# Performance work log

Hardware: AMD Instinct MI355X
Metric: run time of the kernel (lower is better)

The kernel has to match this reference:

```python
import jax, jax.numpy as jnp
import numpy as np

NEG_INF_SCALE = -1e9


def setup_inputs() -> dict:
    key = jax.random.key(0)
    ks = jax.random.split(key, 8)
    B, T, M, D = 64, 1024, 256, 1024
    query = jax.random.normal(ks[0], (B, 1, M), dtype=jnp.float32)
    keys = jax.random.normal(ks[1], (B, T, M), dtype=jnp.float32)
    values = jax.random.normal(ks[2], (B, T, D), dtype=jnp.float32)
    mask = jax.random.randint(ks[3], (B, 1, T), 0, 2).astype(jnp.float32)
    # MLP params (scaled like torch default init ~ 1/sqrt(fan_in))
    W1 = jax.random.normal(ks[4], (4 * M, D), dtype=jnp.float32) / np.sqrt(4 * M)
    b1 = jnp.zeros((D,), dtype=jnp.float32)
    W2 = jax.random.normal(ks[5], (D, D), dtype=jnp.float32) / np.sqrt(D)
    b2 = jnp.zeros((D,), dtype=jnp.float32)
    w_score = jax.random.normal(ks[6], (D, 1), dtype=jnp.float32) / np.sqrt(D)
    b_score = jnp.zeros((1,), dtype=jnp.float32)
    return {"query": query, "keys": keys, "values": values, "mask": mask,
            "W1": W1, "b1": b1, "W2": W2, "b2": b2,
            "w_score": w_score, "b_score": b_score}


def reference(query, keys, values, mask, W1, b1, W2, b2, w_score, b_score):
    # query: [B,1,M] broadcast against keys: [B,T,M]
    q = jnp.broadcast_to(query, keys.shape)
    att_input = jnp.concatenate([q, keys, q - keys, q * keys], axis=-1)  # [B,T,4M]
    h = jax.nn.relu(att_input @ W1 + b1)   # [B,T,D]
    h = jax.nn.relu(h @ W2 + b2)           # [B,T,D]
    score = h @ w_score + b_score          # [B,T,1]
    logits = jnp.swapaxes(score, 1, 2)     # [B,1,T]
    logits = logits + mask * NEG_INF_SCALE
    attn = jax.nn.softmax(logits, axis=-1)  # [B,1,T]
    out = jnp.matmul(attn, values)          # [B,1,D]
    return out
```

## Files before the change

### kernel.cpp

```cpp
#include <hip/hip_runtime.h>

#define DEV __device__ __forceinline__

typedef __attribute__((ext_vector_type(4))) float f32x4;
typedef __attribute__((ext_vector_type(8))) short short8;
typedef __attribute__((ext_vector_type(4))) short s16x4;
typedef __attribute__((ext_vector_type(4))) float f32x4v;

DEV short f2bf(float f) {
  union { float f; unsigned u; } v; v.f = f;
  unsigned r = (v.u + 0x7FFFu + ((v.u >> 16) & 1u)) >> 16;
  return (short)r;
}

DEV void gload16(const void* g, void* l) {
  __builtin_amdgcn_global_load_lds(
      (const __attribute__((address_space(1))) void*)g,
      (__attribute__((address_space(3))) void*)l, 16, 0, 0);
}

#define BAR() __builtin_amdgcn_s_barrier()
#define LGKMW(n)                                              \
  {                                                           \
    asm volatile("s_waitcnt lgkmcnt(" #n ")" ::: "memory");   \
    __builtin_amdgcn_sched_barrier(0);                        \
  }
#define VMW(n)                                                \
  {                                                           \
    asm volatile("s_waitcnt vmcnt(" #n ")" ::: "memory");     \
    __builtin_amdgcn_sched_barrier(0);                        \
  }

#define RD_A(pb, qrt)                                                          \
  _Pragma("unroll") for (int m_ = 0; m_ < 4; ++m_) {                           \
    af[m_][0] = *(const short8*)&lds[(pb) + aoff0 + ((qrt) * 4 + m_) * 1024];  \
    af[m_][1] = *(const short8*)&lds[(pb) + aoff1 + ((qrt) * 4 + m_) * 1024];  \
  }
#define RD_B(pb, nh)                                                             \
  _Pragma("unroll") for (int n_ = 0; n_ < 2; ++n_) {                             \
    bf[nh][n_][0] = *(const short8*)&lds[(pb) + boff0 + ((nh) * 2 + n_) * 1024]; \
    bf[nh][n_][1] = *(const short8*)&lds[(pb) + boff1 + ((nh) * 2 + n_) * 1024]; \
  }
#define MFMA_Q(mq, nh)                                                           \
  __builtin_amdgcn_s_setprio(1);                                                 \
  _Pragma("unroll") for (int m_ = 0; m_ < 4; ++m_) {                             \
    _Pragma("unroll") for (int n_ = 0; n_ < 2; ++n_) {                           \
      acc[(mq) * 4 + m_][(nh) * 2 + n_] =                                        \
          __builtin_amdgcn_mfma_f32_16x16x32_bf16(                               \
              bf[nh][n_][0], af[m_][0], acc[(mq) * 4 + m_][(nh) * 2 + n_], 0, 0, \
              0);                                                                \
      acc[(mq) * 4 + m_][(nh) * 2 + n_] =                                        \
          __builtin_amdgcn_mfma_f32_16x16x32_bf16(                               \
              bf[nh][n_][1], af[m_][1], acc[(mq) * 4 + m_][(nh) * 2 + n_], 0, 0, \
              0);                                                                \
    }                                                                            \
  }                                                                              \
  __builtin_amdgcn_s_setprio(0);

struct FullTag { static constexpr bool value = true; };
struct LastTag { static constexpr bool value = false; };


__global__ __launch_bounds__(256) void k_prep_keys(const float* __restrict__ k,
                                                   short* __restrict__ o) {
  int i = (blockIdx.x * 256 + threadIdx.x) * 8;
  f32x4v v0 = *(const f32x4v*)(k + i);
  f32x4v v1 = *(const f32x4v*)(k + i + 4);
  short8 s;
  s[0] = f2bf(v0[0]); s[1] = f2bf(v0[1]); s[2] = f2bf(v0[2]); s[3] = f2bf(v0[3]);
  s[4] = f2bf(v1[0]); s[5] = f2bf(v1[1]); s[6] = f2bf(v1[2]); s[7] = f2bf(v1[3]);
  *(short8*)(o + i) = s;
}

__global__ __launch_bounds__(256) void k_prep_w2t(const float* __restrict__ w2,
                                                  short* __restrict__ w2t) {
  __shared__ float tile[64][65];
  const int k0 = blockIdx.x * 64, n0 = blockIdx.y * 64;
  const int a = threadIdx.x & 63, q = threadIdx.x >> 6;
#pragma unroll
  for (int i = 0; i < 16; ++i) {
    int kk = i * 4 + q;
    tile[kk][a] = w2[(size_t)(k0 + kk) * 1024 + n0 + a];
  }
  __syncthreads();
#pragma unroll
  for (int i = 0; i < 16; ++i) {
    int nn = i * 4 + q;
    w2t[(size_t)(n0 + nn) * 1024 + k0 + a] = f2bf(tile[a][nn]);
  }
}

__global__ __launch_bounds__(256) void k_prep_wkt(const float* __restrict__ w1,
                                                  const float* __restrict__ query,
                                                  const float* __restrict__ b1,
                                                  short* __restrict__ wkt,
                                                  float* __restrict__ biasb) {
  __shared__ short tile[64][257];
  __shared__ float redm[64][4];
  const int b = blockIdx.x, d0 = blockIdx.y * 64;
  const int d = threadIdx.x & 63, mq = threadIdx.x >> 6;
  float bacc = 0.f;
#pragma unroll 4
  for (int i = 0; i < 64; ++i) {
    int m = i * 4 + mq;
    float qv = query[b * 256 + m];
    float wa = w1[(size_t)m * 1024 + d0 + d];
    float wb = w1[(size_t)(256 + m) * 1024 + d0 + d];
    float wc = w1[(size_t)(512 + m) * 1024 + d0 + d];
    float wd = w1[(size_t)(768 + m) * 1024 + d0 + d];
    tile[d][m] = f2bf(wb - wc + qv * wd);
    bacc += qv * (wa + wc);
  }
  redm[d][mq] = bacc;
  __syncthreads();
  const int m = threadIdx.x;
  for (int dd = 0; dd < 64; ++dd)
    wkt[((size_t)b * 1024 + d0 + dd) * 256 + m] = tile[dd][m];
  if (threadIdx.x < 64) {
    int dd = threadIdx.x;
    biasb[b * 1024 + d0 + dd] =
        redm[dd][0] + redm[dd][1] + redm[dd][2] + redm[dd][3] + b1[d0 + dd];
  }
}


template <int MODE>
__global__ __launch_bounds__(512) void k_gemm8(const short* __restrict__ A,
                                               const short* __restrict__ B,
                                               const float* __restrict__ bias,
                                               const float* __restrict__ wscore,
                                               short* __restrict__ hout,
                                               float* __restrict__ spart) {
  __shared__ short lds[65536];
  constexpr int SK = (MODE == 1) ? 256 : 1024;
  constexpr int KT = (MODE == 1) ? 4 : 16;

  const int tid = threadIdx.x;
  const int bx = blockIdx.x;
  const int L = (bx & 7) * 128 + (bx >> 3);

  const short *Ab, *Bb;
  const float *biasp, *wsp = nullptr;
  short* houtp = nullptr;
  int rt, ct;
  if constexpr (MODE == 1) {
    const int b = L >> 4;
    rt = (L >> 2) & 3; ct = L & 3;
    Ab = A + ((size_t)b * 1024 + rt * 256) * 256;
    Bb = B + ((size_t)b * 1024 + ct * 256) * 256;
    biasp = bias + b * 1024 + ct * 256;
    houtp = hout + ((size_t)(b * 1024 + rt * 256)) * 1024 + ct * 256;
  } else {
    rt = L >> 2; ct = L & 3;
    Ab = A + (size_t)rt * 256 * 1024;
    Bb = B + (size_t)ct * 256 * 1024;
    biasp = bias + ct * 256;
    wsp = wscore + ct * 256;
  }

  const int c0 = tid, c1 = 512 + tid;
  const int r0 = c0 >> 3, k0 = ((c0 & 7) ^ (r0 & 7)) * 8;
  const int r1 = c1 >> 3, k1 = ((c1 & 7) ^ (r1 & 7)) * 8;

  auto STAGE = [&](const short* gb, int kt, int half, int ldsb) {
    gload16(gb + (size_t)(half * 128 + r0) * SK + kt * 64 + k0, &lds[ldsb + c0 * 8]);
    gload16(gb + (size_t)(half * 128 + r1) * SK + kt * 64 + k1, &lds[ldsb + c1 * 8]);
  };

  const int lane = tid & 63, l15 = lane & 15, l4 = lane >> 4;
  const int wid = tid >> 6, wr = wid >> 2, wc = wid & 3;
  const int aoff0 = wr * 8192 + l15 * 64 + ((l4 ^ (l15 & 7)) * 8);
  const int aoff1 = wr * 8192 + l15 * 64 + (((4 + l4) ^ (l15 & 7)) * 8);
  const int boff0 = 16384 + (wc >> 1) * 8192 + (wc & 1) * 4096 + l15 * 64 +
                    ((l4 ^ (l15 & 7)) * 8);
  const int boff1 = 16384 + (wc >> 1) * 8192 + (wc & 1) * 4096 + l15 * 64 +
                    (((4 + l4) ^ (l15 & 7)) * 8);

  f32x4 acc[8][4];
#pragma unroll
  for (int m = 0; m < 8; ++m)
#pragma unroll
    for (int n = 0; n < 4; ++n) acc[m][n] = f32x4{0.f, 0.f, 0.f, 0.f};
  short8 af[4][2];
  short8 bf[2][2][2];

  STAGE(Ab, 0, 0, 0);
  STAGE(Ab, 0, 1, 8192);
  STAGE(Bb, 0, 0, 16384);
  STAGE(Bb, 0, 1, 24576);
  STAGE(Ab, 1, 0, 32768);
  STAGE(Ab, 1, 1, 40960);
  VMW(4);
  BAR();

  auto body = [&](int t, auto tag) {
    constexpr bool FULL = decltype(tag)::value;
    const int p = (t & 1) << 15;
    const int q = p ^ 32768;
    RD_A(p, 0); RD_B(p, 0); RD_B(p, 1);
    STAGE(Bb, t + 1, 0, q + 16384);
    BAR(); LGKMW(4); MFMA_Q(0, 0); BAR();
    STAGE(Bb, t + 1, 1, q + 24576);
    BAR(); LGKMW(0); MFMA_Q(0, 1); BAR();
    RD_A(p, 1);
    if constexpr (FULL) STAGE(Bb, t + 2, 0, p + 16384);
    BAR(); LGKMW(0); MFMA_Q(1, 1); BAR();
    if constexpr (FULL) STAGE(Bb, t + 2, 1, p + 24576);
    BAR();
    MFMA_Q(1, 0);
    if constexpr (FULL) { VMW(4); } else { VMW(0); }
    BAR();
    RD_A(q, 0); RD_B(q, 0); RD_B(q, 1);
    if constexpr (FULL) STAGE(Ab, t + 2, 0, p + 0);
    BAR(); LGKMW(4); MFMA_Q(0, 0); BAR();
    if constexpr (FULL) STAGE(Ab, t + 2, 1, p + 8192);
    BAR(); LGKMW(0); MFMA_Q(0, 1); BAR();
    RD_A(q, 1);
    BAR(); LGKMW(0); MFMA_Q(1, 1); BAR();
    if constexpr (FULL) { STAGE(Ab, t + 3, 0, q + 0); STAGE(Ab, t + 3, 1, q + 8192); }
    BAR();
    MFMA_Q(1, 0);
    if constexpr (FULL) { VMW(4); }
    BAR();
  };

#pragma nounroll
  for (int i = 0; i < KT / 2 - 1; ++i) body(2 * i, FullTag{});
  body(KT - 2, LastTag{});

  if constexpr (MODE == 1) {
    float bv[4][4];
#pragma unroll
    for (int n = 0; n < 4; ++n)
#pragma unroll
      for (int r2 = 0; r2 < 4; ++r2) bv[n][r2] = biasp[wc * 64 + n * 16 + l4 * 4 + r2];
#pragma unroll
    for (int m = 0; m < 8; ++m) {
      int row = wr * 128 + m * 16 + l15;
#pragma unroll
      for (int n = 0; n < 4; ++n) {
        s16x4 pk;
#pragma unroll
        for (int r2 = 0; r2 < 4; ++r2)
          pk[r2] = f2bf(fmaxf(acc[m][n][r2] + bv[n][r2], 0.f));
        *(s16x4*)&houtp[(size_t)row * 1024 + wc * 64 + n * 16 + l4 * 4] = pk;
      }
    }
  } else {
    float bv[4][4], wv[4][4];
#pragma unroll
    for (int n = 0; n < 4; ++n)
#pragma unroll
      for (int r2 = 0; r2 < 4; ++r2) {
        int c = wc * 64 + n * 16 + l4 * 4 + r2;
        bv[n][r2] = biasp[c];
        wv[n][r2] = wsp[c];
      }
    float* so = spart + ((size_t)(ct * 4 + wc) << 16) + rt * 256 + wr * 128;
#pragma unroll
    for (int m = 0; m < 8; ++m) {
      float s = 0.f;
#pragma unroll
      for (int n = 0; n < 4; ++n)
#pragma unroll
        for (int r2 = 0; r2 < 4; ++r2)
          s += fmaxf(acc[m][n][r2] + bv[n][r2], 0.f) * wv[n][r2];
      s += __shfl_xor(s, 16);
      s += __shfl_xor(s, 32);
      if (lane < 16) so[m * 16 + l15] = s;
    }
  }
}


__global__ __launch_bounds__(256) void k_softmax(const float* __restrict__ spart,
                                                 const float* __restrict__ mask,
                                                 const float* __restrict__ bscore,
                                                 float* __restrict__ attn) {
  const int b = blockIdx.x, tid = threadIdx.x;
  __shared__ float sm[1024];
  __shared__ float red[8];
  const float bs = bscore[0];
  float lmax = -3.0e38f;
  for (int t = tid; t < 1024; t += 256) {
    float s = bs;
#pragma unroll
    for (int c = 0; c < 16; ++c) s += spart[(size_t)c * 65536 + b * 1024 + t];
    float lg = s + mask[b * 1024 + t] * (-1e9f);
    sm[t] = lg;
    lmax = fmaxf(lmax, lg);
  }
  for (int o = 32; o; o >>= 1) lmax = fmaxf(lmax, __shfl_xor(lmax, o));
  const int wid = tid >> 6, lane = tid & 63;
  if (lane == 0) red[wid] = lmax;
  __syncthreads();
  float bmax = fmaxf(fmaxf(red[0], red[1]), fmaxf(red[2], red[3]));
  float lsum = 0.f;
  for (int t = tid; t < 1024; t += 256) {
    float e = __expf(sm[t] - bmax);
    sm[t] = e;
    lsum += e;
  }
  for (int o = 32; o; o >>= 1) lsum += __shfl_xor(lsum, o);
  __syncthreads();
  if (lane == 0) red[wid] = lsum;
  __syncthreads();
  float inv = 1.0f / (red[0] + red[1] + red[2] + red[3]);
  for (int t = tid; t < 1024; t += 256) attn[b * 1024 + t] = sm[t] * inv;
}

__global__ __launch_bounds__(256) void k_out(const float* __restrict__ attn,
                                             const float* __restrict__ values,
                                             float* __restrict__ part) {
  const int b = blockIdx.x >> 3, ts = blockIdx.x & 7;
  const int tid = threadIdx.x;
  __shared__ float at[128];
  if (tid < 128) at[tid] = attn[b * 1024 + ts * 128 + tid];
  __syncthreads();
  const float* vb = values + ((size_t)b * 1024 + ts * 128) * 1024 + tid * 4;
  f32x4 acc = {0.f, 0.f, 0.f, 0.f};
#pragma unroll 8
  for (int t = 0; t < 128; ++t) {
    f32x4v v = *(const f32x4v*)(vb + (size_t)t * 1024);
    float a = at[t];
    acc[0] += a * v[0]; acc[1] += a * v[1]; acc[2] += a * v[2]; acc[3] += a * v[3];
  }
  *(f32x4*)(part + ((size_t)(b * 8 + ts)) * 1024 + tid * 4) = acc;
}

__global__ __launch_bounds__(256) void k_red(const float* __restrict__ part,
                                             float* __restrict__ out) {
  const int b = blockIdx.x;
  const int c4 = threadIdx.x * 4;
  f32x4 s = {0.f, 0.f, 0.f, 0.f};
#pragma unroll
  for (int ts = 0; ts < 8; ++ts) {
    f32x4v v = *(const f32x4v*)(part + ((size_t)(b * 8 + ts)) * 1024 + c4);
    s[0] += v[0]; s[1] += v[1]; s[2] += v[2]; s[3] += v[3];
  }
  *(f32x4*)(out + b * 1024 + c4) = s;
}


extern "C" void kernel_launch(void* const* d_in, const int* in_sizes, int n_in,
                              void* d_out, int out_size, void* d_ws, size_t ws_size,
                              hipStream_t stream) {
  const float* query  = (const float*)d_in[0];
  const float* keys   = (const float*)d_in[1];
  const float* values = (const float*)d_in[2];
  const float* mask   = (const float*)d_in[3];
  const float* W1     = (const float*)d_in[4];
  const float* b1     = (const float*)d_in[5];
  const float* W2     = (const float*)d_in[6];
  const float* b2     = (const float*)d_in[7];
  const float* wscore = (const float*)d_in[8];
  const float* bscore = (const float*)d_in[9];
  float* out = (float*)d_out;

  char* ws = (char*)d_ws;
  short* keysb = (short*)(ws);
  short* wkt   = (short*)(ws + 33554432ull);
  short* w2t   = (short*)(ws + 67108864ull);
  float* biasb = (float*)(ws + 69206016ull);
  short* h1    = (short*)(ws + 69468160ull);
  float* spart = (float*)(ws + 203685888ull);
  float* attn  = (float*)(ws + 207880192ull);
  float* part  = (float*)(ws + 208142336ull);

  k_prep_keys<<<8192, 256, 0, stream>>>(keys, keysb);
  k_prep_w2t<<<dim3(16, 16), 256, 0, stream>>>(W2, w2t);
  k_prep_wkt<<<dim3(64, 16), 256, 0, stream>>>(W1, query, b1, wkt, biasb);

  k_gemm8<1><<<1024, 512, 0, stream>>>(keysb, wkt, biasb, nullptr, h1, nullptr);
  k_gemm8<2><<<1024, 512, 0, stream>>>(h1, w2t, b2, wscore, nullptr, spart);

  k_softmax<<<64, 256, 0, stream>>>(spart, mask, bscore, attn);
  k_out<<<512, 256, 0, stream>>>(attn, values, part);
  k_red<<<64, 256, 0, stream>>>(part, out);
}
```

Baseline: 282.7 us.

## Double-buffer fragment registers and reorder GEMM pipeline to overlap LDS reads with MFMA

```diff
diff --git a/kernel.cpp b/kernel.cpp
--- a/kernel.cpp
+++ b/kernel.cpp
@@ -20,6 +20,7 @@
 }
 
 #define BAR() __builtin_amdgcn_s_barrier()
+#define SB0() __builtin_amdgcn_sched_barrier(0)
 #define LGKMW(n)                                              \
   {                                                           \
     asm volatile("s_waitcnt lgkmcnt(" #n ")" ::: "memory");   \
@@ -31,28 +32,28 @@
     __builtin_amdgcn_sched_barrier(0);                        \
   }
 
-#define RD_A(pb, qrt)                                                          \
+#define RD_A(AF, B, qrt)                                                       \
   _Pragma("unroll") for (int m_ = 0; m_ < 4; ++m_) {                           \
-    af[m_][0] = *(const short8*)&lds[(pb) + aoff0 + ((qrt) * 4 + m_) * 1024];  \
-    af[m_][1] = *(const short8*)&lds[(pb) + aoff1 + ((qrt) * 4 + m_) * 1024];  \
-  }
-#define RD_B(pb, nh)                                                             \
+    AF[m_][0] = *(const short8*)&lds[(B) + aoff0 + (qrt) * 4096 + m_ * 1024];  \
+    AF[m_][1] = *(const short8*)&lds[(B) + aoff1 + (qrt) * 4096 + m_ * 1024];  \
+  }
+#define RD_B(BF, B, nh)                                                          \
   _Pragma("unroll") for (int n_ = 0; n_ < 2; ++n_) {                             \
-    bf[nh][n_][0] = *(const short8*)&lds[(pb) + boff0 + ((nh) * 2 + n_) * 1024]; \
-    bf[nh][n_][1] = *(const short8*)&lds[(pb) + boff1 + ((nh) * 2 + n_) * 1024]; \
-  }
-#define MFMA_Q(mq, nh)                                                           \
+    BF[n_][0] = *(const short8*)&lds[(B) + 16384 + (nh) * 8192 + n_ * 4096 +     \
+                                     boff0];                                     \
+    BF[n_][1] = *(const short8*)&lds[(B) + 16384 + (nh) * 8192 + n_ * 4096 +     \
+                                     boff1];                                     \
+  }
+#define MFMA_Q(mq, nh, AF, BF)                                                   \
   __builtin_amdgcn_s_setprio(1);                                                 \
   _Pragma("unroll") for (int m_ = 0; m_ < 4; ++m_) {                             \
     _Pragma("unroll") for (int n_ = 0; n_ < 2; ++n_) {                           \
       acc[(mq) * 4 + m_][(nh) * 2 + n_] =                                        \
           __builtin_amdgcn_mfma_f32_16x16x32_bf16(                               \
-              bf[nh][n_][0], af[m_][0], acc[(mq) * 4 + m_][(nh) * 2 + n_], 0, 0, \
-              0);                                                                \
+              BF[n_][0], AF[m_][0], acc[(mq) * 4 + m_][(nh) * 2 + n_], 0, 0, 0); \
       acc[(mq) * 4 + m_][(nh) * 2 + n_] =                                        \
           __builtin_amdgcn_mfma_f32_16x16x32_bf16(                               \
-              bf[nh][n_][1], af[m_][1], acc[(mq) * 4 + m_][(nh) * 2 + n_], 0, 0, \
-              0);                                                                \
+              BF[n_][1], AF[m_][1], acc[(mq) * 4 + m_][(nh) * 2 + n_], 0, 0, 0); \
     }                                                                            \
   }                                                                              \
   __builtin_amdgcn_s_setprio(0);
@@ -134,6 +135,7 @@
   __shared__ short lds[65536];
   constexpr int SK = (MODE == 1) ? 256 : 1024;
   constexpr int KT = (MODE == 1) ? 4 : 16;
+  constexpr int P = 0, Q = 32768;
 
   const int tid = threadIdx.x;
   const int bx = blockIdx.x;
@@ -171,57 +173,81 @@
   const int wid = tid >> 6, wr = wid >> 2, wc = wid & 3;
   const int aoff0 = wr * 8192 + l15 * 64 + ((l4 ^ (l15 & 7)) * 8);
   const int aoff1 = wr * 8192 + l15 * 64 + (((4 + l4) ^ (l15 & 7)) * 8);
-  const int boff0 = 16384 + (wc >> 1) * 8192 + (wc & 1) * 4096 + l15 * 64 +
-                    ((l4 ^ (l15 & 7)) * 8);
-  const int boff1 = 16384 + (wc >> 1) * 8192 + (wc & 1) * 4096 + l15 * 64 +
-                    (((4 + l4) ^ (l15 & 7)) * 8);
+  const int boff0 = wc * 1024 + l15 * 64 + ((l4 ^ (l15 & 7)) * 8);
+  const int boff1 = wc * 1024 + l15 * 64 + (((4 + l4) ^ (l15 & 7)) * 8);
 
   f32x4 acc[8][4];
 #pragma unroll
   for (int m = 0; m < 8; ++m)
 #pragma unroll
     for (int n = 0; n < 4; ++n) acc[m][n] = f32x4{0.f, 0.f, 0.f, 0.f};
-  short8 af[4][2];
-  short8 bf[2][2][2];
-
-  STAGE(Ab, 0, 0, 0);
-  STAGE(Ab, 0, 1, 8192);
-  STAGE(Bb, 0, 0, 16384);
-  STAGE(Bb, 0, 1, 24576);
-  STAGE(Ab, 1, 0, 32768);
-  STAGE(Ab, 1, 1, 40960);
-  VMW(4);
+  short8 afA[4][2], afB[4][2];
+  short8 bfA[2][2], bfB[2][2];
+
+  STAGE(Ab, 0, 0, P + 0);
+  STAGE(Ab, 0, 1, P + 8192);
+  STAGE(Bb, 0, 0, P + 16384);
+  STAGE(Bb, 0, 1, P + 24576);
+  STAGE(Ab, 1, 0, Q + 0);
+  STAGE(Ab, 1, 1, Q + 8192);
+  VMW(0);
   BAR();
+  RD_A(afA, P, 0);
+  RD_A(afB, P, 1);
+  RD_B(bfA, P, 0);
 
   auto body = [&](int t, auto tag) {
     constexpr bool FULL = decltype(tag)::value;
-    const int p = (t & 1) << 15;
-    const int q = p ^ 32768;
-    RD_A(p, 0); RD_B(p, 0); RD_B(p, 1);
-    STAGE(Bb, t + 1, 0, q + 16384);
-    BAR(); LGKMW(4); MFMA_Q(0, 0); BAR();
-    STAGE(Bb, t + 1, 1, q + 24576);
-    BAR(); LGKMW(0); MFMA_Q(0, 1); BAR();
-    RD_A(p, 1);
-    if constexpr (FULL) STAGE(Bb, t + 2, 0, p + 16384);
-    BAR(); LGKMW(0); MFMA_Q(1, 1); BAR();
-    if constexpr (FULL) STAGE(Bb, t + 2, 1, p + 24576);
-    BAR();
-    MFMA_Q(1, 0);
-    if constexpr (FULL) { VMW(4); } else { VMW(0); }
-    BAR();
-    RD_A(q, 0); RD_B(q, 0); RD_B(q, 1);
-    if constexpr (FULL) STAGE(Ab, t + 2, 0, p + 0);
-    BAR(); LGKMW(4); MFMA_Q(0, 0); BAR();
-    if constexpr (FULL) STAGE(Ab, t + 2, 1, p + 8192);
-    BAR(); LGKMW(0); MFMA_Q(0, 1); BAR();
-    RD_A(q, 1);
-    BAR(); LGKMW(0); MFMA_Q(1, 1); BAR();
-    if constexpr (FULL) { STAGE(Ab, t + 3, 0, q + 0); STAGE(Ab, t + 3, 1, q + 8192); }
-    BAR();
-    MFMA_Q(1, 0);
-    if constexpr (FULL) { VMW(4); }
-    BAR();
+    LGKMW(0);
+    MFMA_Q(0, 0, afA, bfA);
+    STAGE(Bb, t + 1, 0, Q + 16384);
+    VMW(6);
+    BAR();
+    RD_B(bfB, P, 1);
+    SB0();
+    MFMA_Q(1, 0, afB, bfA);
+    STAGE(Bb, t + 1, 1, Q + 24576);
+    BAR();
+    LGKMW(0);
+    MFMA_Q(1, 1, afB, bfB);
+    if constexpr (FULL) STAGE(Ab, t + 2, 0, P + 0);
+    if constexpr (FULL) { VMW(4); } else { VMW(2); }
+    BAR();
+    RD_B(bfA, Q, 0);
+    SB0();
+    MFMA_Q(0, 1, afA, bfB);
+    RD_A(afA, Q, 0);
+    if constexpr (FULL) STAGE(Ab, t + 2, 1, P + 8192);
+    BAR();
+    LGKMW(0);
+    RD_A(afB, Q, 1);
+    SB0();
+    MFMA_Q(0, 0, afA, bfA);
+    if constexpr (FULL) STAGE(Bb, t + 2, 0, P + 16384);
+    if constexpr (FULL) { VMW(6); } else { VMW(0); }
+    BAR();
+    LGKMW(0);
+    RD_B(bfB, Q, 1);
+    SB0();
+    MFMA_Q(1, 0, afB, bfA);
+    if constexpr (FULL) STAGE(Bb, t + 2, 1, P + 24576);
+    BAR();
+    LGKMW(0);
+    MFMA_Q(1, 1, afB, bfB);
+    if constexpr (FULL) STAGE(Ab, t + 3, 0, Q + 0);
+    if constexpr (FULL) VMW(4);
+    BAR();
+    if constexpr (FULL) {
+      RD_B(bfA, P, 0);
+      RD_A(afB, P, 1);
+      SB0();
+    }
+    MFMA_Q(0, 1, afA, bfB);
+    if constexpr (FULL) {
+      RD_A(afA, P, 0);
+      STAGE(Ab, t + 3, 1, Q + 8192);
+      BAR();
+    }
   };
 
 #pragma nounroll
@@ -233,7 +259,8 @@
 #pragma unroll
     for (int n = 0; n < 4; ++n)
 #pragma unroll
-      for (int r2 = 0; r2 < 4; ++r2) bv[n][r2] = biasp[wc * 64 + n * 16 + l4 * 4 + r2];
+      for (int r2 = 0; r2 < 4; ++r2)
+        bv[n][r2] = biasp[(n >> 1) * 128 + (n & 1) * 64 + wc * 16 + l4 * 4 + r2];
 #pragma unroll
     for (int m = 0; m < 8; ++m) {
       int row = wr * 128 + m * 16 + l15;
@@ -243,7 +270,8 @@
 #pragma unroll
         for (int r2 = 0; r2 < 4; ++r2)
           pk[r2] = f2bf(fmaxf(acc[m][n][r2] + bv[n][r2], 0.f));
-        *(s16x4*)&houtp[(size_t)row * 1024 + wc * 64 + n * 16 + l4 * 4] = pk;
+        *(s16x4*)&houtp[(size_t)row * 1024 + (n >> 1) * 128 + (n & 1) * 64 +
+                        wc * 16 + l4 * 4] = pk;
       }
     }
   } else {
@@ -252,7 +280,7 @@
     for (int n = 0; n < 4; ++n)
 #pragma unroll
       for (int r2 = 0; r2 < 4; ++r2) {
-        int c = wc * 64 + n * 16 + l4 * 4 + r2;
+        int c = (n >> 1) * 128 + (n & 1) * 64 + wc * 16 + l4 * 4 + r2;
         bv[n][r2] = biasp[c];
         wv[n][r2] = wsp[c];
       }
```

Measured after the change: 335.3 us. 1.19x slower.

## Replace 256x256 8-wave GEMM with 128x256 4-wave double-buffered tile

Applied to the files above, without the earlier changes.

```diff
diff --git a/kernel.cpp b/kernel.cpp
--- a/kernel.cpp
+++ b/kernel.cpp
@@ -30,35 +30,6 @@
     asm volatile("s_waitcnt vmcnt(" #n ")" ::: "memory");     \
     __builtin_amdgcn_sched_barrier(0);                        \
   }
-
-#define RD_A(pb, qrt)                                                          \
-  _Pragma("unroll") for (int m_ = 0; m_ < 4; ++m_) {                           \
-    af[m_][0] = *(const short8*)&lds[(pb) + aoff0 + ((qrt) * 4 + m_) * 1024];  \
-    af[m_][1] = *(const short8*)&lds[(pb) + aoff1 + ((qrt) * 4 + m_) * 1024];  \
-  }
-#define RD_B(pb, nh)                                                             \
-  _Pragma("unroll") for (int n_ = 0; n_ < 2; ++n_) {                             \
-    bf[nh][n_][0] = *(const short8*)&lds[(pb) + boff0 + ((nh) * 2 + n_) * 1024]; \
-    bf[nh][n_][1] = *(const short8*)&lds[(pb) + boff1 + ((nh) * 2 + n_) * 1024]; \
-  }
-#define MFMA_Q(mq, nh)                                                           \
-  __builtin_amdgcn_s_setprio(1);                                                 \
-  _Pragma("unroll") for (int m_ = 0; m_ < 4; ++m_) {                             \
-    _Pragma("unroll") for (int n_ = 0; n_ < 2; ++n_) {                           \
-      acc[(mq) * 4 + m_][(nh) * 2 + n_] =                                        \
-          __builtin_amdgcn_mfma_f32_16x16x32_bf16(                               \
-              bf[nh][n_][0], af[m_][0], acc[(mq) * 4 + m_][(nh) * 2 + n_], 0, 0, \
-              0);                                                                \
-      acc[(mq) * 4 + m_][(nh) * 2 + n_] =                                        \
-          __builtin_amdgcn_mfma_f32_16x16x32_bf16(                               \
-              bf[nh][n_][1], af[m_][1], acc[(mq) * 4 + m_][(nh) * 2 + n_], 0, 0, \
-              0);                                                                \
-    }                                                                            \
-  }                                                                              \
-  __builtin_amdgcn_s_setprio(0);
-
-struct FullTag { static constexpr bool value = true; };
-struct LastTag { static constexpr bool value = false; };
 
 
 __global__ __launch_bounds__(256) void k_prep_keys(const float* __restrict__ k,
@@ -125,125 +96,116 @@
 
 
 template <int MODE>
-__global__ __launch_bounds__(512) void k_gemm8(const short* __restrict__ A,
-                                               const short* __restrict__ B,
-                                               const float* __restrict__ bias,
-                                               const float* __restrict__ wscore,
-                                               short* __restrict__ hout,
-                                               float* __restrict__ spart) {
-  __shared__ short lds[65536];
+__global__ __launch_bounds__(256, 2) void k_gemm(const short* __restrict__ A,
+                                                 const short* __restrict__ B,
+                                                 const float* __restrict__ bias,
+                                                 const float* __restrict__ wscore,
+                                                 short* __restrict__ hout,
+                                                 float* __restrict__ spart) {
+  __shared__ short lds[24576];
   constexpr int SK = (MODE == 1) ? 256 : 1024;
-  constexpr int KT = (MODE == 1) ? 4 : 16;
+  constexpr int KT = (MODE == 1) ? 8 : 32;
 
   const int tid = threadIdx.x;
   const int bx = blockIdx.x;
-  const int L = (bx & 7) * 128 + (bx >> 3);
+  const int L = (bx & 7) * 256 + (bx >> 3);
 
   const short *Ab, *Bb;
   const float *biasp, *wsp = nullptr;
   short* houtp = nullptr;
   int rt, ct;
   if constexpr (MODE == 1) {
-    const int b = L >> 4;
-    rt = (L >> 2) & 3; ct = L & 3;
-    Ab = A + ((size_t)b * 1024 + rt * 256) * 256;
+    const int b = L >> 5;
+    rt = (L >> 2) & 7; ct = L & 3;
+    Ab = A + ((size_t)b * 1024 + rt * 128) * 256;
     Bb = B + ((size_t)b * 1024 + ct * 256) * 256;
     biasp = bias + b * 1024 + ct * 256;
-    houtp = hout + ((size_t)(b * 1024 + rt * 256)) * 1024 + ct * 256;
+    houtp = hout + ((size_t)(b * 1024 + rt * 128)) * 1024 + ct * 256;
   } else {
     rt = L >> 2; ct = L & 3;
-    Ab = A + (size_t)rt * 256 * 1024;
+    Ab = A + (size_t)rt * 128 * 1024;
     Bb = B + (size_t)ct * 256 * 1024;
     biasp = bias + ct * 256;
     wsp = wscore + ct * 256;
   }
 
-  const int c0 = tid, c1 = 512 + tid;
-  const int r0 = c0 >> 3, k0 = ((c0 & 7) ^ (r0 & 7)) * 8;
-  const int r1 = c1 >> 3, k1 = ((c1 & 7) ^ (r1 & 7)) * 8;
-
-  auto STAGE = [&](const short* gb, int kt, int half, int ldsb) {
-    gload16(gb + (size_t)(half * 128 + r0) * SK + kt * 64 + k0, &lds[ldsb + c0 * 8]);
-    gload16(gb + (size_t)(half * 128 + r1) * SK + kt * 64 + k1, &lds[ldsb + c1 * 8]);
+  int gA[2], dA[2], gB[4], dB[4];
+#pragma unroll
+  for (int j = 0; j < 2; ++j) {
+    int s = tid + j * 256, row = s >> 2, c = (s & 3) ^ ((row >> 1) & 3);
+    gA[j] = row * SK + c * 8;
+    dA[j] = s * 8;
+  }
+#pragma unroll
+  for (int j = 0; j < 4; ++j) {
+    int s = tid + j * 256, row = s >> 2, c = (s & 3) ^ ((row >> 1) & 3);
+    gB[j] = row * SK + c * 8;
+    dB[j] = 4096 + s * 8;
+  }
+
+  auto STAGE = [&](int kt, int buf) {
+#pragma unroll
+    for (int j = 0; j < 2; ++j) gload16(Ab + gA[j] + kt * 32, &lds[buf + dA[j]]);
+#pragma unroll
+    for (int j = 0; j < 4; ++j) gload16(Bb + gB[j] + kt * 32, &lds[buf + dB[j]]);
   };
 
-  const int lane = tid & 63, l15 = lane & 15, l4 = lane >> 4;
-  const int wid = tid >> 6, wr = wid >> 2, wc = wid & 3;
-  const int aoff0 = wr * 8192 + l15 * 64 + ((l4 ^ (l15 & 7)) * 8);
-  const int aoff1 = wr * 8192 + l15 * 64 + (((4 + l4) ^ (l15 & 7)) * 8);
-  const int boff0 = 16384 + (wc >> 1) * 8192 + (wc & 1) * 4096 + l15 * 64 +
-                    ((l4 ^ (l15 & 7)) * 8);
-  const int boff1 = 16384 + (wc >> 1) * 8192 + (wc & 1) * 4096 + l15 * 64 +
-                    (((4 + l4) ^ (l15 & 7)) * 8);
+  const int lane = tid & 63, l15 = lane & 15, l4 = lane >> 4, wc = tid >> 6;
+  const int swz = (l4 ^ ((l15 >> 1) & 3)) * 8;
+  const int aoff = l15 * 32 + swz;
+  const int boff = 4096 + wc * 512 + l15 * 32 + swz;
 
   f32x4 acc[8][4];
 #pragma unroll
   for (int m = 0; m < 8; ++m)
 #pragma unroll
     for (int n = 0; n < 4; ++n) acc[m][n] = f32x4{0.f, 0.f, 0.f, 0.f};
-  short8 af[4][2];
-  short8 bf[2][2][2];
-
-  STAGE(Ab, 0, 0, 0);
-  STAGE(Ab, 0, 1, 8192);
-  STAGE(Bb, 0, 0, 16384);
-  STAGE(Bb, 0, 1, 24576);
-  STAGE(Ab, 1, 0, 32768);
-  STAGE(Ab, 1, 1, 40960);
-  VMW(4);
-  BAR();
-
-  auto body = [&](int t, auto tag) {
-    constexpr bool FULL = decltype(tag)::value;
-    const int p = (t & 1) << 15;
-    const int q = p ^ 32768;
-    RD_A(p, 0); RD_B(p, 0); RD_B(p, 1);
-    STAGE(Bb, t + 1, 0, q + 16384);
-    BAR(); LGKMW(4); MFMA_Q(0, 0); BAR();
-    STAGE(Bb, t + 1, 1, q + 24576);
-    BAR(); LGKMW(0); MFMA_Q(0, 1); BAR();
-    RD_A(p, 1);
-    if constexpr (FULL) STAGE(Bb, t + 2, 0, p + 16384);
-    BAR(); LGKMW(0); MFMA_Q(1, 1); BAR();
-    if constexpr (FULL) STAGE(Bb, t + 2, 1, p + 24576);
+
+  STAGE(0, 0);
+#pragma unroll 2
+  for (int kt = 0; kt < KT; ++kt) {
+    const int cur = (kt & 1) * 12288;
+    if (kt + 1 < KT) {
+      STAGE(kt + 1, 12288 - cur);
+      VMW(6);
+    } else {
+      VMW(0);
+    }
     BAR();
-    MFMA_Q(1, 0);
-    if constexpr (FULL) { VMW(4); } else { VMW(0); }
+    short8 af[8], bf[4];
+#pragma unroll
+    for (int m = 0; m < 8; ++m) af[m] = *(const short8*)&lds[cur + aoff + m * 512];
+#pragma unroll
+    for (int n = 0; n < 4; ++n) bf[n] = *(const short8*)&lds[cur + boff + n * 2048];
+    LGKMW(0);
     BAR();
-    RD_A(q, 0); RD_B(q, 0); RD_B(q, 1);
-    if constexpr (FULL) STAGE(Ab, t + 2, 0, p + 0);
-    BAR(); LGKMW(4); MFMA_Q(0, 0); BAR();
-    if constexpr (FULL) STAGE(Ab, t + 2, 1, p + 8192);
-    BAR(); LGKMW(0); MFMA_Q(0, 1); BAR();
-    RD_A(q, 1);
-    BAR(); LGKMW(0); MFMA_Q(1, 1); BAR();
-    if constexpr (FULL) { STAGE(Ab, t + 3, 0, q + 0); STAGE(Ab, t + 3, 1, q + 8192); }
-    BAR();
-    MFMA_Q(1, 0);
-    if constexpr (FULL) { VMW(4); }
-    BAR();
-  };
-
-#pragma nounroll
-  for (int i = 0; i < KT / 2 - 1; ++i) body(2 * i, FullTag{});
-  body(KT - 2, LastTag{});
+    __builtin_amdgcn_s_setprio(1);
+#pragma unroll
+    for (int m = 0; m < 8; ++m)
+#pragma unroll
+      for (int n = 0; n < 4; ++n)
+        acc[m][n] = __builtin_amdgcn_mfma_f32_16x16x32_bf16(bf[n], af[m],
+                                                            acc[m][n], 0, 0, 0);
+    __builtin_amdgcn_s_setprio(0);
+  }
 
   if constexpr (MODE == 1) {
     float bv[4][4];
 #pragma unroll
     for (int n = 0; n < 4; ++n)
 #pragma unroll
-      for (int r2 = 0; r2 < 4; ++r2) bv[n][r2] = biasp[wc * 64 + n * 16 + l4 * 4 + r2];
+      for (int r2 = 0; r2 < 4; ++r2)
+        bv[n][r2] = biasp[n * 64 + wc * 16 + l4 * 4 + r2];
 #pragma unroll
     for (int m = 0; m < 8; ++m) {
-      int row = wr * 128 + m * 16 + l15;
+      int row = m * 16 + l15;
 #pragma unroll
       for (int n = 0; n < 4; ++n) {
         s16x4 pk;
 #pragma unroll
         for (int r2 = 0; r2 < 4; ++r2)
           pk[r2] = f2bf(fmaxf(acc[m][n][r2] + bv[n][r2], 0.f));
-        *(s16x4*)&houtp[(size_t)row * 1024 + wc * 64 + n * 16 + l4 * 4] = pk;
+        *(s16x4*)&houtp[(size_t)row * 1024 + n * 64 + wc * 16 + l4 * 4] = pk;
       }
     }
   } else {
@@ -252,11 +214,11 @@
     for (int n = 0; n < 4; ++n)
 #pragma unroll
       for (int r2 = 0; r2 < 4; ++r2) {
-        int c = wc * 64 + n * 16 + l4 * 4 + r2;
+        int c = n * 64 + wc * 16 + l4 * 4 + r2;
         bv[n][r2] = biasp[c];
         wv[n][r2] = wsp[c];
       }
-    float* so = spart + ((size_t)(ct * 4 + wc) << 16) + rt * 256 + wr * 128;
+    float* so = spart + ((size_t)(ct * 4 + wc) << 16) + rt * 128;
 #pragma unroll
     for (int m = 0; m < 8; ++m) {
       float s = 0.f;
@@ -371,8 +333,8 @@
   k_prep_w2t<<<dim3(16, 16), 256, 0, stream>>>(W2, w2t);
   k_prep_wkt<<<dim3(64, 16), 256, 0, stream>>>(W1, query, b1, wkt, biasb);
 
-  k_gemm8<1><<<1024, 512, 0, stream>>>(keysb, wkt, biasb, nullptr, h1, nullptr);
-  k_gemm8<2><<<1024, 512, 0, stream>>>(h1, w2t, b2, wscore, nullptr, spart);
+  k_gemm<1><<<2048, 256, 0, stream>>>(keysb, wkt, biasb, nullptr, h1, nullptr);
+  k_gemm<2><<<2048, 256, 0, stream>>>(h1, w2t, b2, wscore, nullptr, spart);
 
   k_softmax<<<64, 256, 0, stream>>>(spart, mask, bscore, attn);
   k_out<<<512, 256, 0, stream>>>(attn, values, part);
```

New measurement: 293.3 us. 1.04x slower.
